# Kernel optimization log

Measured on AMD Instinct MI355X. Metric: run time of the kernel, lower is better.

The kernel has to match this reference:

```python
import jax, jax.numpy as jnp
import numpy as np

K = 16  # neighborhood size


def _eigen_ratio(pts, k):
    """pts: [B, N, 3] -> ratio lambda_max / lambda_mid per point, [B, N]."""
    pts = pts[..., :3]
    # pairwise squared distances [B, N, N]
    sq = jnp.sum(pts * pts, axis=-1)  # [B, N]
    d2 = sq[:, :, None] + sq[:, None, :] - 2.0 * jnp.einsum('bnd,bmd->bnm', pts, pts)
    # k nearest neighbors (self included, as in KNN(x, x))
    _, idx = jax.lax.top_k(-d2, k)  # idx: [B, N, k] int32
    # gather neighbor coordinates: [B, N, k, 3]
    neighbors = jax.vmap(lambda p, i: p[i])(pts, idx)
    mean = jnp.mean(neighbors, axis=2, keepdims=True)
    diff = neighbors - mean  # [B, N, k, 3]
    # covariance = mean over k of outer products -> [B, N, 3, 3]
    cov = jnp.einsum('bnki,bnkj->bnij', diff, diff) / k
    ev = jnp.linalg.eigvalsh(cov)  # ascending: [..., 3]
    return ev[..., 2] / ev[..., 1]


def setup_inputs() -> dict:
    key = jax.random.key(0)
    kx, ky = jax.random.split(key)
    x = jax.random.normal(kx, (2, 8192, 3), dtype=jnp.float32)
    y = jax.random.normal(ky, (2, 8192, 3), dtype=jnp.float32)
    return {"x": x, "y": y}


def reference(x, y):
    er1 = _eigen_ratio(x, K)  # [B, N]
    er2 = _eigen_ratio(y, K)
    res = jnp.mean((er1 - er2) ** 2, axis=-1)  # mean over points
    return jnp.mean(res)  # reduction='mean' over batch
```

## Files before the change

kernel.cpp:

```cpp
#include <hip/hip_runtime.h>
#include <hip/hip_bf16.h>
#include <math.h>

#define NPTS   8192
#define KNN    16
#define G      16
#define NCELL  (G * G * G)
#define NCHUNK 128
#define NPART  4

__constant__ float c_B[17] = {
    -1e30f,
    -1.5341205f, -1.1503494f, -0.8871466f, -0.6744898f, -0.4887764f,
    -0.3186394f, -0.1573107f,  0.0f,        0.1573107f,  0.3186394f,
     0.4887764f,  0.6744898f,  0.8871466f,  1.1503494f,  1.5341205f,
     1e30f
};

__device__ __forceinline__ int cellOf(float v) {
    int c = 0;
#pragma unroll
    for (int i = 1; i <= 15; ++i) c += (v >= c_B[i]) ? 1 : 0;
    return c;
}

__device__ __forceinline__ int spread3(int v) {
    v = (v | (v << 4)) & 0x0C3;
    v = (v | (v << 2)) & 0x249;
    return v;
}

__device__ __forceinline__ int mortonCell(float px, float py, float pz) {
    return (spread3(cellOf(px)) << 2) | (spread3(cellOf(py)) << 1) | spread3(cellOf(pz));
}

__device__ __forceinline__ float dpp_prev_f(float v) {
    int r = __builtin_amdgcn_update_dpp(0, __float_as_int(v), 0x111, 0xF, 0xF, false);
    return __int_as_float(r);
}
__device__ __forceinline__ int dpp_prev_i(int v) {
    return __builtin_amdgcn_update_dpp(0, v, 0x111, 0xF, 0xF, false);
}

__device__ __forceinline__ float sum16(float v) {
    int b;
    b = __builtin_amdgcn_update_dpp(0, __float_as_int(v), 0xB1, 0xF, 0xF, false);
    v += __int_as_float(b);
    b = __builtin_amdgcn_update_dpp(0, __float_as_int(v), 0x4E, 0xF, 0xF, false);
    v += __int_as_float(b);
    b = __builtin_amdgcn_update_dpp(0, __float_as_int(v), 0x141, 0xF, 0xF, false);
    v += __int_as_float(b);
    b = __builtin_amdgcn_update_dpp(0, __float_as_int(v), 0x140, 0xF, 0xF, false);
    v += __int_as_float(b);
    return v;
}

__global__ __launch_bounds__(256) void count_kernel(
    const float* __restrict__ x, const float* __restrict__ y,
    unsigned int* __restrict__ cellcnt) {

    __shared__ unsigned int h[NCELL];
    const int tid   = threadIdx.x;
    const int cloud = blockIdx.x >> 2;
    const int part  = blockIdx.x & 3;
    const float* __restrict__ src = (cloud < 2 ? x : y) + (size_t)(cloud & 1) * NPTS * 3;

    for (int i = tid; i < NCELL; i += 256) h[i] = 0;
    __syncthreads();
#pragma unroll
    for (int k = 0; k < 8; ++k) {
        int p = (part << 11) | (k << 8) | tid;
        atomicAdd(&h[mortonCell(src[3 * p], src[3 * p + 1], src[3 * p + 2])], 1u);
    }
    __syncthreads();
    unsigned int* cc = cellcnt + (cloud * NPART + part) * NCELL;
    for (int i = tid; i < NCELL; i += 256) cc[i] = h[i];
}

__global__ __launch_bounds__(1024) void scan_kernel(unsigned int* __restrict__ cellcnt) {
    __shared__ unsigned int scanbuf[1024];
    const int tid = threadIdx.x;
    unsigned int* cc = cellcnt + blockIdx.x * (NPART * NCELL);

    unsigned int v[NPART][4], csum[4];
    unsigned int ssum = 0;
#pragma unroll
    for (int j = 0; j < 4; ++j) {
        int cell = 4 * tid + j;
        unsigned int s = 0;
#pragma unroll
        for (int p = 0; p < NPART; ++p) { v[p][j] = cc[p * NCELL + cell]; s += v[p][j]; }
        csum[j] = s; ssum += s;
    }
    scanbuf[tid] = ssum;
    __syncthreads();
    for (int d = 1; d < 1024; d <<= 1) {
        unsigned int a = scanbuf[tid];
        unsigned int w = (tid >= d) ? scanbuf[tid - d] : 0;
        __syncthreads();
        scanbuf[tid] = a + w;
        __syncthreads();
    }
    unsigned int run = scanbuf[tid] - ssum;
#pragma unroll
    for (int j = 0; j < 4; ++j) {
        int cell = 4 * tid + j;
        unsigned int pr = run;
#pragma unroll
        for (int p = 0; p < NPART; ++p) { cc[p * NCELL + cell] = pr; pr += v[p][j]; }
        run += csum[j];
    }
}

__global__ __launch_bounds__(256) void scatter_kernel(
    const float* __restrict__ x, const float* __restrict__ y,
    unsigned int* __restrict__ cellcnt,
    float4* __restrict__ Ps, unsigned short* __restrict__ origids) {

    const int tid   = threadIdx.x;
    const int cloud = blockIdx.x >> 2;
    const int part  = blockIdx.x & 3;
    const float* __restrict__ src = (cloud < 2 ? x : y) + (size_t)(cloud & 1) * NPTS * 3;
    unsigned int* cc = cellcnt + (cloud * NPART + part) * NCELL;

#pragma unroll
    for (int k = 0; k < 8; ++k) {
        int p = (part << 11) | (k << 8) | tid;
        float px = src[3 * p], py = src[3 * p + 1], pz = src[3 * p + 2];
        int c = mortonCell(px, py, pz);
        unsigned int pos = atomicAdd(&cc[c], 1u);
        Ps[(cloud << 13) + pos] = make_float4(-2.f * px, -2.f * py, -2.f * pz,
                                              px * px + py * py + pz * pz);
        origids[(cloud << 13) + pos] = (unsigned short)p;
    }
}

__global__ __launch_bounds__(256) void aabb_kernel(
    const float4* __restrict__ Ps, float* __restrict__ aabbG ) {

    const int tid  = threadIdx.x;
    const int lane = tid & 63;
    const int w    = (blockIdx.x << 2) | (tid >> 6);
    const int cloud = w >> 7;
    const int c     = w & 127;

    float4 f = Ps[(cloud << 13) | (c << 6) | lane];
    float px = -0.5f * f.x, py = -0.5f * f.y, pz = -0.5f * f.z;
    float lx = px, hx = px, ly = py, hy = py, lz = pz, hz = pz;
#pragma unroll
    for (int s = 1; s < 64; s <<= 1) {
        lx = fminf(lx, __shfl_xor(lx, s)); hx = fmaxf(hx, __shfl_xor(hx, s));
        ly = fminf(ly, __shfl_xor(ly, s)); hy = fmaxf(hy, __shfl_xor(hy, s));
        lz = fminf(lz, __shfl_xor(lz, s)); hz = fmaxf(hz, __shfl_xor(hz, s));
    }
    if (lane == 0) {
        float* ab = aabbG + cloud * (6 * NCHUNK);
        ab[0 * NCHUNK + c] = lx; ab[1 * NCHUNK + c] = hx;
        ab[2 * NCHUNK + c] = ly; ab[3 * NCHUNK + c] = hy;
        ab[4 * NCHUNK + c] = lz; ab[5 * NCHUNK + c] = hz;
    }
}

__global__ __launch_bounds__(256) void knn_cov_kernel(
    const float4* __restrict__ Ps, const unsigned short* __restrict__ origids,
    const float* __restrict__ aabbG, float* __restrict__ cov) {

    __shared__ float sA[6 * NCHUNK];

    const int tid  = threadIdx.x;
    const int lane = tid & 63;
    const int wv   = tid >> 6;
    const int cloud = blockIdx.x >> 11;
    const int s     = ((blockIdx.x << 2) | wv) & (NPTS - 1);

    for (int i = tid; i < 6 * NCHUNK; i += 256) sA[i] = aabbG[cloud * (6 * NCHUNK) + i];
    __syncthreads();

    const float4* __restrict__ Pc = Ps + (cloud << 13);
    const float4 qp = Pc[s];
    const float sqq = qp.w;
    const float qx = -0.5f * qp.x, qy = -0.5f * qp.y, qz = -0.5f * qp.z;
    const int co = s >> 6;

    float bval[2];
#pragma unroll
    for (int g = 0; g < 2; ++g) {
        int c = (g << 6) | lane;
        float dxl = fmaxf(0.f, fmaxf(sA[c] - qx, qx - sA[NCHUNK + c]));
        float dyl = fmaxf(0.f, fmaxf(sA[2 * NCHUNK + c] - qy, qy - sA[3 * NCHUNK + c]));
        float dzl = fmaxf(0.f, fmaxf(sA[4 * NCHUNK + c] - qz, qz - sA[5 * NCHUNK + c]));
        bval[g] = dxl * dxl + dyl * dyl + dzl * dzl;
    }
    unsigned long long rem0 = ~0ull, rem1 = ~0ull;
    if (co < 64) rem0 &= ~(1ull << co); else rem1 &= ~(1ull << (co - 64));

    auto dual_argmin = [&](unsigned long long live0, unsigned long long live1,
                           int& cidA, int& cidB, bool& hasA, bool& hasB) {
        unsigned int k0 = ((live0 >> lane) & 1)
            ? ((__float_as_uint(bval[0]) & 0xFFFFFF80u) | (unsigned)lane) : 0xFFFFFFFFu;
        unsigned int k1 = ((live1 >> lane) & 1)
            ? ((__float_as_uint(bval[1]) & 0xFFFFFF80u) | (unsigned)(64 + lane)) : 0xFFFFFFFFu;
        unsigned int a = min(k0, k1), b = max(k0, k1);
#pragma unroll
        for (int w = 1; w < 64; w <<= 1) {
            unsigned int oa = __shfl_xor(a, w);
            unsigned int ob = __shfl_xor(b, w);
            unsigned int mn = min(a, oa), mx = max(a, oa);
            unsigned int c2 = (a < oa) ? b : ob;
            a = mn; b = min(mx, c2);
        }
        hasA = (a != 0xFFFFFFFFu); cidA = (int)(a & 127u);
        hasB = (b != 0xFFFFFFFFu); cidB = (int)(b & 127u);
    };
    auto clear_rem = [&](int cid) {
        if (cid < 64) rem0 &= ~(1ull << cid); else rem1 &= ~(1ull << (cid - 64));
    };
    auto bound_of = [&](int cid) {
        return __int_as_float(__builtin_amdgcn_readlane(
            __float_as_int(bval[cid >> 6]), cid & 63));
    };

    int pA, pB; bool hA, hB;
    dual_argmin(rem0, rem1, pA, pB, hA, hB);
    clear_rem(pA); clear_rem(pB);
    float4 pfA = Pc[(pA << 6) | lane];
    float4 pfB = Pc[(pB << 6) | lane];

    float valV, thr;
    int   idxV;
    {
        int pos = (co << 6) | lane;
        float4 f = Pc[pos];
        float k = fmaf(qx, f.x, fmaf(qy, f.y, fmaf(qz, f.z, sqq + f.w)));
        int p = pos;
#pragma unroll
        for (int size = 2; size <= 64; size <<= 1) {
#pragma unroll
            for (int stride = size >> 1; stride >= 1; stride >>= 1) {
                float ok = __shfl_xor(k, stride);
                int   op = __shfl_xor(p, stride);
                bool up = ((lane & size) == 0);
                bool lower = ((lane & stride) == 0);
                bool want_min = (up == lower);
                bool take = want_min ? (ok < k) : (ok > k);
                k = take ? ok : k;
                p = take ? op : p;
            }
        }
        valV = __shfl(k, lane & 15);
        idxV = __shfl(p, lane & 15);
        thr  = __shfl(k, 15);
    }

    auto process = [&](float4 f, int cid) {
        float d2 = fmaf(qx, f.x, fmaf(qy, f.y, fmaf(qz, f.z, sqq + f.w)));
        unsigned long long m = __ballot(d2 < thr);
        if (m) {
            do {
                int li = __builtin_ctzll(m); m &= m - 1;
                float sv = __int_as_float(
                    __builtin_amdgcn_readlane(__float_as_int(d2), li));
                int sj = (cid << 6) | li;
                float pv = dpp_prev_f(valV);
                int   pi = dpp_prev_i(idxV);
                bool keep  = (valV <= sv);
                bool fromv = ((lane & 15) == 0) || (pv <= sv);
                float nv = keep ? valV : (fromv ? sv : pv);
                int   ni = keep ? idxV : (fromv ? sj : pi);
                valV = nv; idxV = ni;
            } while (m);
            thr = __int_as_float(__builtin_amdgcn_readlane(__float_as_int(valV), 15));
        }
    };

    if (bound_of(pA) < thr) process(pfA, pA);
    if (bound_of(pB) < thr) process(pfB, pB);

    for (;;) {
        unsigned long long live0 = rem0 & __ballot(bval[0] < thr);
        unsigned long long live1 = rem1 & __ballot(bval[1] < thr);
        if (!(live0 | live1)) break;

        int cidA, cidB; bool hasA, hasB;
        dual_argmin(live0, live1, cidA, cidB, hasA, hasB);
        clear_rem(cidA);
        if (hasB) clear_rem(cidB);

        float4 fA = Pc[(cidA << 6) | lane];
        float4 fB;
        if (hasB) fB = Pc[(cidB << 6) | lane];

        process(fA, cidA);
        if (hasB && bound_of(cidB) < thr) process(fB, cidB);
    }

    float4 nf = Pc[idxV];
    float nx = -0.5f * nf.x, ny = -0.5f * nf.y, nz = -0.5f * nf.z;

    const float invk = 1.0f / KNN;
    float mx = sum16(nx) * invk;
    float my = sum16(ny) * invk;
    float mz = sum16(nz) * invk;

    float dx = nx - mx, dy = ny - my, dz = nz - mz;
    float c00 = sum16(dx * dx), c01 = sum16(dx * dy), c02 = sum16(dx * dz);
    float c11 = sum16(dy * dy), c12 = sum16(dy * dz), c22 = sum16(dz * dz);

    if (lane == 0) {
        int orig = origids[(cloud << 13) + s];
        float* cp = cov + ((size_t)(cloud << 13) + orig) * 6;
        cp[0] = c00 * invk; cp[1] = c01 * invk; cp[2] = c02 * invk;
        cp[3] = c11 * invk; cp[4] = c12 * invk; cp[5] = c22 * invk;
    }
}

__device__ double eig_ratio(const float* __restrict__ cp) {
    double a00 = cp[0], a01 = cp[1], a02 = cp[2];
    double a11 = cp[3], a12 = cp[4], a22 = cp[5];

    double qm = (a00 + a11 + a22) * (1.0 / 3.0);
    double p1 = a01 * a01 + a02 * a02 + a12 * a12;
    double b00 = a00 - qm, b11 = a11 - qm, b22 = a22 - qm;
    double p2 = b00 * b00 + b11 * b11 + b22 * b22 + 2.0 * p1;

    if (p2 <= 0.0) return 1.0;
    double p = sqrt(p2 * (1.0 / 6.0));
    double inv = 1.0 / p;
    double m00 = b00 * inv, m11 = b11 * inv, m22 = b22 * inv;
    double m01 = a01 * inv, m02 = a02 * inv, m12 = a12 * inv;
    double detB = m00 * (m11 * m22 - m12 * m12)
                - m01 * (m01 * m22 - m12 * m02)
                + m02 * (m01 * m12 - m11 * m02);
    double r = 0.5 * detB;
    r = fmin(1.0, fmax(-1.0, r));
    double phi = acos(r) * (1.0 / 3.0);
    double e1 = qm + 2.0 * p * cos(phi);
    double e3 = qm + 2.0 * p * cos(phi + 2.0943951023931953);
    double e2 = 3.0 * qm - e1 - e3;
    return e1 / e2;
}

__global__ __launch_bounds__(256) void eigred_kernel(const float* __restrict__ cov,
                                                     double* __restrict__ partial) {
    __shared__ double sb[256];
    const int i = blockIdx.x * 256 + threadIdx.x;
    double r1 = eig_ratio(cov + (size_t)i * 6);
    double r2 = eig_ratio(cov + (size_t)(2 * NPTS + i) * 6);
    double d = r1 - r2;
    sb[threadIdx.x] = d * d;
    __syncthreads();
    for (int s2 = 128; s2 > 0; s2 >>= 1) {
        if (threadIdx.x < s2) sb[threadIdx.x] += sb[threadIdx.x + s2];
        __syncthreads();
    }
    if (threadIdx.x == 0) partial[blockIdx.x] = sb[0];
}

__global__ __launch_bounds__(64) void final_kernel(const double* __restrict__ partial,
                                                   float* __restrict__ out) {
    double v = partial[threadIdx.x];
#pragma unroll
    for (int w = 1; w < 64; w <<= 1) v += __shfl_xor(v, w);
    if (threadIdx.x == 0) out[0] = (float)(v / (double)(2 * NPTS));
}

extern "C" void kernel_launch(void* const* d_in, const int* in_sizes, int n_in,
                              void* d_out, int out_size, void* d_ws, size_t ws_size,
                              hipStream_t stream) {
    const float* x = (const float*)d_in[0];
    const float* y = (const float*)d_in[1];
    char* ws = (char*)d_ws;

    float4*         Ps      = (float4*)(ws);
    unsigned short* origids = (unsigned short*)(ws + 524288);
    float*          aabbG   = (float*)(ws + 589824);
    float*          cov     = (float*)(ws + 602112);
    unsigned int*   cellcnt = (unsigned int*)(ws + 1388544);
    double*         partial = (double*)(ws + 1650688);
    float*          out     = (float*)d_out;

    count_kernel<<<4 * NPART, 256, 0, stream>>>(x, y, cellcnt);
    scan_kernel<<<4, 1024, 0, stream>>>(cellcnt);
    scatter_kernel<<<4 * NPART, 256, 0, stream>>>(x, y, cellcnt, Ps, origids);
    aabb_kernel<<<128, 256, 0, stream>>>(Ps, aabbG);
    knn_cov_kernel<<<8192, 256, 0, stream>>>(Ps, origids, aabbG, cov);
    eigred_kernel<<<64, 256, 0, stream>>>(cov, partial);
    final_kernel<<<1, 64, 0, stream>>>(partial, out);
}
```

Measured before the change: 95.68 us.

## Fuse eigen-ratio into KNN kernel, use one-wave blocks, fast path for few live chunks

The KNN/covariance kernel now computes the eigenvalue ratio in place and writes one float per point, which removes the eigred kernel and the 6-float covariance round trip. The final reduction becomes a single 1024-thread block. The KNN kernel switches to 64-thread blocks, one query per block, and reads AABBs straight from global memory instead of staging them in LDS behind a barrier. When at most two candidate chunks remain live, a ctz-based pick replaces the shuffle argmin. The costs are double-precision eigen math on every lane of the KNN kernel and more, smaller blocks.

```diff
diff --git a/kernel.cpp b/kernel.cpp
--- a/kernel.cpp
+++ b/kernel.cpp
@@ -161,22 +161,17 @@
     }
 }
 
-__global__ __launch_bounds__(256) void knn_cov_kernel(
+__global__ __launch_bounds__(64) void knn_cov_kernel(
     const float4* __restrict__ Ps, const unsigned short* __restrict__ origids,
-    const float* __restrict__ aabbG, float* __restrict__ cov) {
-
-    __shared__ float sA[6 * NCHUNK];
-
-    const int tid  = threadIdx.x;
-    const int lane = tid & 63;
-    const int wv   = tid >> 6;
-    const int cloud = blockIdx.x >> 11;
-    const int s     = ((blockIdx.x << 2) | wv) & (NPTS - 1);
-
-    for (int i = tid; i < 6 * NCHUNK; i += 256) sA[i] = aabbG[cloud * (6 * NCHUNK) + i];
-    __syncthreads();
+    const float* __restrict__ aabbG, float* __restrict__ er) {
+
+    const int lane = threadIdx.x;
+    const int wid  = blockIdx.x;
+    const int cloud = wid >> 13;
+    const int s     = wid & (NPTS - 1);
 
     const float4* __restrict__ Pc = Ps + (cloud << 13);
+    const float* __restrict__ ab = aabbG + cloud * (6 * NCHUNK);
     const float4 qp = Pc[s];
     const float sqq = qp.w;
     const float qx = -0.5f * qp.x, qy = -0.5f * qp.y, qz = -0.5f * qp.z;
@@ -186,16 +181,16 @@
 #pragma unroll
     for (int g = 0; g < 2; ++g) {
         int c = (g << 6) | lane;
-        float dxl = fmaxf(0.f, fmaxf(sA[c] - qx, qx - sA[NCHUNK + c]));
-        float dyl = fmaxf(0.f, fmaxf(sA[2 * NCHUNK + c] - qy, qy - sA[3 * NCHUNK + c]));
-        float dzl = fmaxf(0.f, fmaxf(sA[4 * NCHUNK + c] - qz, qz - sA[5 * NCHUNK + c]));
+        float dxl = fmaxf(0.f, fmaxf(ab[c] - qx, qx - ab[NCHUNK + c]));
+        float dyl = fmaxf(0.f, fmaxf(ab[2 * NCHUNK + c] - qy, qy - ab[3 * NCHUNK + c]));
+        float dzl = fmaxf(0.f, fmaxf(ab[4 * NCHUNK + c] - qz, qz - ab[5 * NCHUNK + c]));
         bval[g] = dxl * dxl + dyl * dyl + dzl * dzl;
     }
     unsigned long long rem0 = ~0ull, rem1 = ~0ull;
     if (co < 64) rem0 &= ~(1ull << co); else rem1 &= ~(1ull << (co - 64));
 
     auto dual_argmin = [&](unsigned long long live0, unsigned long long live1,
-                           int& cidA, int& cidB, bool& hasA, bool& hasB) {
+                           int& cidA, int& cidB, bool& hasB) {
         unsigned int k0 = ((live0 >> lane) & 1)
             ? ((__float_as_uint(bval[0]) & 0xFFFFFF80u) | (unsigned)lane) : 0xFFFFFFFFu;
         unsigned int k1 = ((live1 >> lane) & 1)
@@ -209,7 +204,7 @@
             unsigned int c2 = (a < oa) ? b : ob;
             a = mn; b = min(mx, c2);
         }
-        hasA = (a != 0xFFFFFFFFu); cidA = (int)(a & 127u);
+        cidA = (int)(a & 127u);
         hasB = (b != 0xFFFFFFFFu); cidB = (int)(b & 127u);
     };
     auto clear_rem = [&](int cid) {
@@ -220,8 +215,8 @@
             __float_as_int(bval[cid >> 6]), cid & 63));
     };
 
-    int pA, pB; bool hA, hB;
-    dual_argmin(rem0, rem1, pA, pB, hA, hB);
+    int pA, pB; bool hB;
+    dual_argmin(rem0, rem1, pA, pB, hB);
     clear_rem(pA); clear_rem(pB);
     float4 pfA = Pc[(pA << 6) | lane];
     float4 pfB = Pc[(pB << 6) | lane];
@@ -281,8 +276,16 @@
         unsigned long long live1 = rem1 & __ballot(bval[1] < thr);
         if (!(live0 | live1)) break;
 
-        int cidA, cidB; bool hasA, hasB;
-        dual_argmin(live0, live1, cidA, cidB, hasA, hasB);
+        int cidA, cidB; bool hasB;
+        if (__popcll(live0) + __popcll(live1) <= 2) {
+            if (live0) { cidA = __builtin_ctzll(live0); live0 &= live0 - 1; }
+            else       { cidA = 64 + __builtin_ctzll(live1); live1 &= live1 - 1; }
+            if (live0)      { cidB = __builtin_ctzll(live0); hasB = true; }
+            else if (live1) { cidB = 64 + __builtin_ctzll(live1); hasB = true; }
+            else hasB = false;
+        } else {
+            dual_argmin(live0, live1, cidA, cidB, hasB);
+        }
         clear_rem(cidA);
         if (hasB) clear_rem(cidB);
 
@@ -303,65 +306,57 @@
     float mz = sum16(nz) * invk;
 
     float dx = nx - mx, dy = ny - my, dz = nz - mz;
-    float c00 = sum16(dx * dx), c01 = sum16(dx * dy), c02 = sum16(dx * dz);
-    float c11 = sum16(dy * dy), c12 = sum16(dy * dz), c22 = sum16(dz * dz);
-
-    if (lane == 0) {
-        int orig = origids[(cloud << 13) + s];
-        float* cp = cov + ((size_t)(cloud << 13) + orig) * 6;
-        cp[0] = c00 * invk; cp[1] = c01 * invk; cp[2] = c02 * invk;
-        cp[3] = c11 * invk; cp[4] = c12 * invk; cp[5] = c22 * invk;
-    }
-}
-
-__device__ double eig_ratio(const float* __restrict__ cp) {
-    double a00 = cp[0], a01 = cp[1], a02 = cp[2];
-    double a11 = cp[3], a12 = cp[4], a22 = cp[5];
-
+    float c00 = sum16(dx * dx) * invk, c01 = sum16(dx * dy) * invk, c02 = sum16(dx * dz) * invk;
+    float c11 = sum16(dy * dy) * invk, c12 = sum16(dy * dz) * invk, c22 = sum16(dz * dz) * invk;
+
+    double a00 = c00, a01 = c01, a02 = c02, a11 = c11, a12 = c12, a22 = c22;
     double qm = (a00 + a11 + a22) * (1.0 / 3.0);
     double p1 = a01 * a01 + a02 * a02 + a12 * a12;
     double b00 = a00 - qm, b11 = a11 - qm, b22 = a22 - qm;
     double p2 = b00 * b00 + b11 * b11 + b22 * b22 + 2.0 * p1;
 
-    if (p2 <= 0.0) return 1.0;
-    double p = sqrt(p2 * (1.0 / 6.0));
-    double inv = 1.0 / p;
-    double m00 = b00 * inv, m11 = b11 * inv, m22 = b22 * inv;
-    double m01 = a01 * inv, m02 = a02 * inv, m12 = a12 * inv;
-    double detB = m00 * (m11 * m22 - m12 * m12)
-                - m01 * (m01 * m22 - m12 * m02)
-                + m02 * (m01 * m12 - m11 * m02);
-    double r = 0.5 * detB;
-    r = fmin(1.0, fmax(-1.0, r));
-    double phi = acos(r) * (1.0 / 3.0);
-    double e1 = qm + 2.0 * p * cos(phi);
-    double e3 = qm + 2.0 * p * cos(phi + 2.0943951023931953);
-    double e2 = 3.0 * qm - e1 - e3;
-    return e1 / e2;
-}
-
-__global__ __launch_bounds__(256) void eigred_kernel(const float* __restrict__ cov,
-                                                     double* __restrict__ partial) {
-    __shared__ double sb[256];
-    const int i = blockIdx.x * 256 + threadIdx.x;
-    double r1 = eig_ratio(cov + (size_t)i * 6);
-    double r2 = eig_ratio(cov + (size_t)(2 * NPTS + i) * 6);
-    double d = r1 - r2;
-    sb[threadIdx.x] = d * d;
+    double ratio;
+    if (p2 <= 0.0) {
+        ratio = 1.0;
+    } else {
+        double p = sqrt(p2 * (1.0 / 6.0));
+        double inv = 1.0 / p;
+        double m00 = b00 * inv, m11 = b11 * inv, m22 = b22 * inv;
+        double m01 = a01 * inv, m02 = a02 * inv, m12 = a12 * inv;
+        double detB = m00 * (m11 * m22 - m12 * m12)
+                    - m01 * (m01 * m22 - m12 * m02)
+                    + m02 * (m01 * m12 - m11 * m02);
+        double r = 0.5 * detB;
+        r = fmin(1.0, fmax(-1.0, r));
+        double phi = acos(r) * (1.0 / 3.0);
+        double e1 = qm + 2.0 * p * cos(phi);
+        double e3 = qm + 2.0 * p * cos(phi + 2.0943951023931953);
+        double e2 = 3.0 * qm - e1 - e3;
+        ratio = e1 / e2;
+    }
+
+    if (lane == 0) {
+        int orig = origids[(cloud << 13) + s];
+        er[(cloud << 13) + orig] = (float)ratio;
+    }
+}
+
+__global__ __launch_bounds__(1024) void final_kernel(const float* __restrict__ er,
+                                                     float* __restrict__ out) {
+    __shared__ double sb[1024];
+    double acc = 0.0;
+    const int total = 2 * NPTS;
+    for (int i = threadIdx.x; i < total; i += 1024) {
+        double d = (double)er[i] - (double)er[total + i];
+        acc += d * d;
+    }
+    sb[threadIdx.x] = acc;
     __syncthreads();
-    for (int s2 = 128; s2 > 0; s2 >>= 1) {
+    for (int s2 = 512; s2 > 0; s2 >>= 1) {
         if (threadIdx.x < s2) sb[threadIdx.x] += sb[threadIdx.x + s2];
         __syncthreads();
     }
-    if (threadIdx.x == 0) partial[blockIdx.x] = sb[0];
-}
-
-__global__ __launch_bounds__(64) void final_kernel(const double* __restrict__ partial,
-                                                   float* __restrict__ out) {
-    double v = partial[threadIdx.x];
-#pragma unroll
-    for (int w = 1; w < 64; w <<= 1) v += __shfl_xor(v, w);
-    if (threadIdx.x == 0) out[0] = (float)(v / (double)(2 * NPTS));
+    if (threadIdx.x == 0) out[0] = (float)(sb[0] / (double)total);
 }
 
 extern "C" void kernel_launch(void* const* d_in, const int* in_sizes, int n_in,
@@ -374,16 +369,14 @@
     float4*         Ps      = (float4*)(ws);
     unsigned short* origids = (unsigned short*)(ws + 524288);
     float*          aabbG   = (float*)(ws + 589824);
-    float*          cov     = (float*)(ws + 602112);
-    unsigned int*   cellcnt = (unsigned int*)(ws + 1388544);
-    double*         partial = (double*)(ws + 1650688);
+    float*          er      = (float*)(ws + 602112);
+    unsigned int*   cellcnt = (unsigned int*)(ws + 733184);
     float*          out     = (float*)d_out;
 
     count_kernel<<<4 * NPART, 256, 0, stream>>>(x, y, cellcnt);
     scan_kernel<<<4, 1024, 0, stream>>>(cellcnt);
     scatter_kernel<<<4 * NPART, 256, 0, stream>>>(x, y, cellcnt, Ps, origids);
     aabb_kernel<<<128, 256, 0, stream>>>(Ps, aabbG);
-    knn_cov_kernel<<<8192, 256, 0, stream>>>(Ps, origids, aabbG, cov);
-    eigred_kernel<<<64, 256, 0, stream>>>(cov, partial);
-    final_kernel<<<1, 64, 0, stream>>>(partial, out);
-}
+    knn_cov_kernel<<<4 * NPTS, 64, 0, stream>>>(Ps, origids, aabbG, er);
+    final_kernel<<<1, 1024, 0, stream>>>(er, out);
+}
```

New measurement: 102.3 us. 6.9% more time.
